# Optimization experiments

Measured on AMD Instinct MI355X. Metric: run time of the kernel, lower is better.

Reference implementation:

```python
import jax, jax.numpy as jnp
import numpy as np
from jax import lax

NUM_HEADS = 4
SIDE = 5  # side_dwconv


def setup_inputs() -> dict:
    key = jax.random.key(0)
    ks = jax.random.split(key, 7)
    B, C, H, W = 2, 128, 56, 56
    return {
        "x": jax.random.normal(ks[0], (B, C, H, W), dtype=jnp.float32),
        "qkv_w": jax.random.normal(ks[1], (3 * C, C), dtype=jnp.float32) * 0.02,
        "qkv_b": jax.random.normal(ks[2], (3 * C,), dtype=jnp.float32) * 0.02,
        "lepe_w": jax.random.normal(ks[3], (C, 1, SIDE, SIDE), dtype=jnp.float32) * 0.02,
        "lepe_b": jax.random.normal(ks[4], (C,), dtype=jnp.float32) * 0.02,
        "proj_w": jax.random.normal(ks[5], (C, C), dtype=jnp.float32) * 0.02,
        "proj_b": jax.random.normal(ks[6], (C,), dtype=jnp.float32) * 0.02,
    }


def reference(x, qkv_w, qkv_b, lepe_w, lepe_b, proj_w, proj_b):
    B, C, H, W = x.shape
    nh = NUM_HEADS
    hd = C // nh
    scale = hd ** (-0.5)
    N = H * W

    # 1x1 conv qkv == channel matmul
    qkv = jnp.einsum('oc,bchw->bohw', qkv_w, x) + qkv_b[None, :, None, None]
    q, k, v = jnp.split(qkv, 3, axis=1)  # each [B, C, H, W]

    qr = q.reshape(B, nh, hd, N)
    kr = k.reshape(B, nh, hd, N)
    vr = v.reshape(B, nh, hd, N)

    # attn = q^T k over head_dim -> [B, nh, N, N]
    attn = jnp.einsum('bhdn,bhdm->bhnm', qr, kr) * scale
    attn = jax.nn.softmax(attn, axis=-1)

    # out = attn @ v^T, then permute back to [B, C, H, W]
    out = jnp.einsum('bhnm,bhdm->bhdn', attn, vr).reshape(B, C, H, W)

    # depthwise LePE conv on v, fused with residual add
    pad = SIDE // 2
    lepe = lax.conv_general_dilated(
        v, lepe_w, window_strides=(1, 1), padding=[(pad, pad), (pad, pad)],
        dimension_numbers=('NCHW', 'OIHW', 'NCHW'), feature_group_count=C,
    ) + lepe_b[None, :, None, None]
    out = out + lepe

    # 1x1 conv proj
    out = jnp.einsum('oc,bchw->bohw', proj_w, out) + proj_b[None, :, None, None]
    return out
```

## Files before the change

kernel.cpp:

```cpp
#include <hip/hip_runtime.h>

typedef __bf16 bf16x8 __attribute__((ext_vector_type(8)));
typedef __bf16 bf16x4 __attribute__((ext_vector_type(4)));
typedef float  f32x4  __attribute__((ext_vector_type(4)));

#define NPIX  3136
#define WIMG  56
#define CCH   128
#define NH    4
#define HD    32
#define NSPLIT 4
#define QSCALE 0.2550565470841439f

#if __has_builtin(__builtin_amdgcn_exp2f)
#define FEXP2(x) __builtin_amdgcn_exp2f(x)
#else
#define FEXP2(x) __expf((x) * 0.6931471805599453f)
#endif


__device__ __forceinline__ int perm_inv(int k) {
    return (((k >> 5) & 1) * 2 + ((k >> 2) & 1)) * 16 + (((k >> 3) & 3) * 4) + (k & 3);
}

__global__ __launch_bounds__(256) void k_qkv(
    const float* __restrict__ x, const float* __restrict__ qkv_w,
    const float* __restrict__ qkv_b,
    __bf16* __restrict__ qT, __bf16* __restrict__ kT,
    __bf16* __restrict__ vT, __bf16* __restrict__ vP)
{
    __shared__ __bf16 xl[64][136];
    const int tid = threadIdx.x;
    const int w = tid >> 6, lane = tid & 63;
    const int col = lane & 15, g = lane >> 4;
    const int px0 = blockIdx.x * 64;
    const int slab = blockIdx.y;
    const int b = blockIdx.z;
    const int obase = slab * 128 + w * 32;

    {
        const int px = tid & 63, cq = tid >> 6;
        const float* xp = x + (size_t)b * CCH * NPIX + px0 + px;
        #pragma unroll
        for (int i = 0; i < 8; ++i) {
            const int c0 = cq * 4 + i * 16;
            const float v0 = xp[(size_t)(c0 + 0) * NPIX];
            const float v1 = xp[(size_t)(c0 + 1) * NPIX];
            const float v2 = xp[(size_t)(c0 + 2) * NPIX];
            const float v3 = xp[(size_t)(c0 + 3) * NPIX];
            bf16x4 bv = {(__bf16)v0, (__bf16)v1, (__bf16)v2, (__bf16)v3};
            *(bf16x4*)&xl[px][c0] = bv;
        }
    }
    __syncthreads();

    f32x4 acc[2][4];
    #pragma unroll
    for (int ot = 0; ot < 2; ++ot)
        #pragma unroll
        for (int a = 0; a < 4; ++a) acc[ot][a] = (f32x4){0.f, 0.f, 0.f, 0.f};

    #pragma unroll
    for (int ks = 0; ks < 4; ++ks) {
        const int c0 = ks * 32 + g * 8;
        #pragma unroll
        for (int ot = 0; ot < 2; ++ot) {
            const float* wrow = qkv_w + (size_t)(obase + ot * 16 + col) * CCH + c0;
            const float4 wA = *(const float4*)(wrow);
            const float4 wB = *(const float4*)(wrow + 4);
            bf16x8 af = {(__bf16)wA.x, (__bf16)wA.y, (__bf16)wA.z, (__bf16)wA.w,
                         (__bf16)wB.x, (__bf16)wB.y, (__bf16)wB.z, (__bf16)wB.w};
            #pragma unroll
            for (int a = 0; a < 4; ++a) {
                const bf16x8 bf_ = *(const bf16x8*)&xl[16 * a + col][c0];
                acc[ot][a] = __builtin_amdgcn_mfma_f32_16x16x32_bf16(af, bf_, acc[ot][a], 0, 0, 0);
            }
        }
    }

    #pragma unroll
    for (int ot = 0; ot < 2; ++ot) {
        const int orow = obase + ot * 16 + g * 4;
        const f32x4 bias4 = *(const f32x4*)(qkv_b + orow);
        if (slab == 0) {
            const int o = orow, h = o >> 5, d0 = o & 31;
            __bf16* dst = qT + ((size_t)(b * NH + h) * NPIX) * HD + d0;
            #pragma unroll
            for (int a = 0; a < 4; ++a) {
                const int px = px0 + 16 * a + col;
                bf16x4 v;
                #pragma unroll
                for (int r = 0; r < 4; ++r) v[r] = (__bf16)((acc[ot][a][r] + bias4[r]) * QSCALE);
                *(bf16x4*)(dst + (size_t)px * HD) = v;
            }
        } else if (slab == 1) {
            const int o = orow - 128, h = o >> 5, d0 = o & 31;
            __bf16* dst = kT + ((size_t)(b * NH + h) * NPIX) * HD + d0;
            #pragma unroll
            for (int a = 0; a < 4; ++a) {
                const int s = perm_inv(16 * a + col);
                bf16x4 v;
                #pragma unroll
                for (int r = 0; r < 4; ++r) v[r] = (__bf16)(acc[ot][a][r] + bias4[r]);
                *(bf16x4*)(dst + (size_t)(px0 + s) * HD) = v;
            }
        } else {
            const int c = orow - 256;
            #pragma unroll
            for (int a = 0; a < 4; ++a) {
                const int px = px0 + 16 * a + col;
                const int s = perm_inv(16 * a + col);
                bf16x4 v;
                #pragma unroll
                for (int r = 0; r < 4; ++r) v[r] = (__bf16)(acc[ot][a][r] + bias4[r]);
                *(bf16x4*)(vT + ((size_t)(b * NPIX + px)) * CCH + c) = v;
                #pragma unroll
                for (int r = 0; r < 4; ++r)
                    vP[((size_t)(b * CCH + c + r)) * NPIX + px0 + s] = v[r];
            }
        }
    }
}

__global__ __launch_bounds__(256) void k_attn(
    const __bf16* __restrict__ qT, const __bf16* __restrict__ kT,
    const __bf16* __restrict__ vP,
    __bf16* __restrict__ pO, float* __restrict__ pl)
{
    const int tid = threadIdx.x;
    const int w = tid >> 6, lane = tid & 63;
    const int col = lane & 15, g = lane >> 4;
    const int qt = blockIdx.x * 2 + (w >> 1);
    const int bh = blockIdx.y;
    const int sp = blockIdx.z * 2 + (w & 1);
    const int b = bh >> 2, h = bh & 3;
    const int qbase = qt * 32;
    const size_t headoff = (size_t)bh * NPIX * HD;
    const int c0h = h * HD;

    const bf16x8 aqA = *(const bf16x8*)(qT + headoff + (size_t)(qbase + col) * HD + g * 8);
    const bf16x8 aqB = *(const bf16x8*)(qT + headoff + (size_t)(qbase + 16 + col) * HD + g * 8);

    const __bf16 one = (__bf16)1.0f;
    const bf16x8 ones = {one, one, one, one, one, one, one, one};

    f32x4 O[2][2], Lacc[2];
    #pragma unroll
    for (int i = 0; i < 2; ++i) {
        Lacc[i] = (f32x4){0.f, 0.f, 0.f, 0.f};
        #pragma unroll
        for (int j = 0; j < 2; ++j) O[i][j] = (f32x4){0.f, 0.f, 0.f, 0.f};
    }

    const __bf16* kTh   = kT + headoff;
    const __bf16* vrow0 = vP + (size_t)(b * CCH + c0h + col)      * NPIX;
    const __bf16* vrow1 = vP + (size_t)(b * CCH + c0h + 16 + col) * NPIX;

    const int cs = (49 * sp) >> 2, ce = (49 * (sp + 1)) >> 2;
    const int nch = ce - cs;

#define LOADK(DK, CHUNK) do { const int _k0 = (CHUNK) * 64;                               \
        _Pragma("unroll")                                                                  \
        for (int _c = 0; _c < 4; ++_c)                                                     \
            DK[_c] = *(const bf16x8*)(kTh + (size_t)(_k0 + 16 * _c + col) * HD + g * 8);   \
        } while (0)

    auto compute = [&](const bf16x8* bk, int chunk) {
        const int k0 = chunk * 64;
        const bf16x8 vv00 = *(const bf16x8*)(vrow0 + k0      + g * 8);
        const bf16x8 vv01 = *(const bf16x8*)(vrow0 + k0 + 32 + g * 8);
        const bf16x8 vv10 = *(const bf16x8*)(vrow1 + k0      + g * 8);
        const bf16x8 vv11 = *(const bf16x8*)(vrow1 + k0 + 32 + g * 8);
        const f32x4 z = {0.f, 0.f, 0.f, 0.f};
        #pragma unroll
        for (int qh = 0; qh < 2; ++qh) {
            const bf16x8 aq = qh ? aqB : aqA;
            f32x4 s0 = __builtin_amdgcn_mfma_f32_16x16x32_bf16(bk[0], aq, z, 0, 0, 0);
            f32x4 s1 = __builtin_amdgcn_mfma_f32_16x16x32_bf16(bk[1], aq, z, 0, 0, 0);
            f32x4 s2 = __builtin_amdgcn_mfma_f32_16x16x32_bf16(bk[2], aq, z, 0, 0, 0);
            f32x4 s3 = __builtin_amdgcn_mfma_f32_16x16x32_bf16(bk[3], aq, z, 0, 0, 0);
            bf16x8 P0 = {(__bf16)FEXP2(s0[0]), (__bf16)FEXP2(s0[1]),
                         (__bf16)FEXP2(s0[2]), (__bf16)FEXP2(s0[3]),
                         (__bf16)FEXP2(s1[0]), (__bf16)FEXP2(s1[1]),
                         (__bf16)FEXP2(s1[2]), (__bf16)FEXP2(s1[3])};
            bf16x8 P1 = {(__bf16)FEXP2(s2[0]), (__bf16)FEXP2(s2[1]),
                         (__bf16)FEXP2(s2[2]), (__bf16)FEXP2(s2[3]),
                         (__bf16)FEXP2(s3[0]), (__bf16)FEXP2(s3[1]),
                         (__bf16)FEXP2(s3[2]), (__bf16)FEXP2(s3[3])};
            O[qh][0] = __builtin_amdgcn_mfma_f32_16x16x32_bf16(vv00, P0, O[qh][0], 0, 0, 0);
            O[qh][0] = __builtin_amdgcn_mfma_f32_16x16x32_bf16(vv01, P1, O[qh][0], 0, 0, 0);
            O[qh][1] = __builtin_amdgcn_mfma_f32_16x16x32_bf16(vv10, P0, O[qh][1], 0, 0, 0);
            O[qh][1] = __builtin_amdgcn_mfma_f32_16x16x32_bf16(vv11, P1, O[qh][1], 0, 0, 0);
            Lacc[qh] = __builtin_amdgcn_mfma_f32_16x16x32_bf16(ones, P0, Lacc[qh], 0, 0, 0);
            Lacc[qh] = __builtin_amdgcn_mfma_f32_16x16x32_bf16(ones, P1, Lacc[qh], 0, 0, 0);
        }
    };

    bf16x8 kA[4], kB[4];
    LOADK(kA, cs);
    int cc = cs;
    while (cc + 2 <= ce) {
        LOADK(kB, cc + 1);
        compute(kA, cc);
        LOADK(kA, (cc + 2 < ce) ? cc + 2 : cs);
        compute(kB, cc + 1);
        cc += 2;
    }
    if (cc < ce) compute(kA, cc);
#undef LOADK

    const int t = bh * 98 + qt;
    __bf16* po = pO + ((size_t)t * NSPLIT + sp) * 1024;
    #pragma unroll
    for (int qh = 0; qh < 2; ++qh)
        #pragma unroll
        for (int dh = 0; dh < 2; ++dh) {
            bf16x4 v = {(__bf16)O[qh][dh][0], (__bf16)O[qh][dh][1],
                        (__bf16)O[qh][dh][2], (__bf16)O[qh][dh][3]};
            *(bf16x4*)(po + (qh * 16 + col) * 32 + dh * 16 + g * 4) = v;
        }
    if (g == 0) {
        float* plp = pl + ((size_t)t * NSPLIT + sp) * 32;
        plp[col]      = Lacc[0][0];
        plp[col + 16] = Lacc[1][0];
    }
}

__global__ __launch_bounds__(256) void k_reduce(
    const __bf16* __restrict__ pO, const float* __restrict__ pl,
    const __bf16* __restrict__ vT,
    const float* __restrict__ lepe_w, const float* __restrict__ lepe_b,
    __bf16* __restrict__ attnT)
{
    __shared__ float wl[32][25];
    __shared__ float bl[32];
    const int tid = threadIdx.x;
    const int qt = blockIdx.x, bh = blockIdx.y;
    const int b = bh >> 2, h = bh & 3;
    const int c0h = h * HD;

    for (int i = tid; i < 800; i += 256) ((float*)wl)[i] = lepe_w[c0h * 25 + i];
    if (tid < 32) bl[tid] = lepe_b[c0h + tid];
    __syncthreads();

    const int q = tid >> 3;
    const int cq = (tid & 7) * 4;
    const size_t t = (size_t)bh * 98 + qt;

    float lt = 0.f;
    float o[4] = {0.f, 0.f, 0.f, 0.f};
    #pragma unroll
    for (int s = 0; s < NSPLIT; ++s) {
        lt += pl[(t * NSPLIT + s) * 32 + q];
        const bf16x4 pv = *(const bf16x4*)(pO + (t * NSPLIT + s) * 1024 + q * 32 + cq);
        #pragma unroll
        for (int i = 0; i < 4; ++i) o[i] += (float)pv[i];
    }
    const float linv = 1.0f / lt;
    #pragma unroll
    for (int i = 0; i < 4; ++i) o[i] = o[i] * linv + bl[cq + i];

    const int px = qt * 32 + q;
    const int py = px / WIMG, pxx = px % WIMG;
    const __bf16* vtb = vT + ((size_t)b * NPIX) * CCH + c0h + cq;
    #pragma unroll
    for (int dy = 0; dy < 5; ++dy) {
        const int yy = py + dy - 2;
        if (yy < 0 || yy >= WIMG) continue;
        #pragma unroll
        for (int dx = 0; dx < 5; ++dx) {
            const int xx = pxx + dx - 2;
            if (xx < 0 || xx >= WIMG) continue;
            const bf16x4 vv = *(const bf16x4*)(vtb + (size_t)(yy * WIMG + xx) * CCH);
            const int tap = dy * 5 + dx;
            #pragma unroll
            for (int i = 0; i < 4; ++i) o[i] += (float)vv[i] * wl[cq + i][tap];
        }
    }
    bf16x4 ov = {(__bf16)o[0], (__bf16)o[1], (__bf16)o[2], (__bf16)o[3]};
    *(bf16x4*)(attnT + ((size_t)(b * NPIX + px)) * CCH + c0h + cq) = ov;
}

__global__ __launch_bounds__(256) void k_proj(
    const __bf16* __restrict__ attnT, const float* __restrict__ proj_w,
    const float* __restrict__ proj_b, float* __restrict__ out)
{
    const int tid = threadIdx.x;
    const int w = tid >> 6, lane = tid & 63;
    const int col = lane & 15, g = lane >> 4;
    const int px0 = blockIdx.x * 32 + (w >> 1) * 16;
    const int obase = blockIdx.y * 32 + (w & 1) * 16;
    const int b = blockIdx.z;

    const float* wrow = proj_w + (size_t)(obase + col) * CCH;
    const __bf16* abase = attnT + (size_t)(b * NPIX + px0) * CCH;

    f32x4 acc = {0.f, 0.f, 0.f, 0.f};
    #pragma unroll
    for (int ks = 0; ks < 4; ++ks) {
        const int c0 = ks * 32 + g * 8;
        const float4 wA = *(const float4*)(wrow + c0);
        const float4 wB = *(const float4*)(wrow + c0 + 4);
        bf16x8 af = {(__bf16)wA.x, (__bf16)wA.y, (__bf16)wA.z, (__bf16)wA.w,
                     (__bf16)wB.x, (__bf16)wB.y, (__bf16)wB.z, (__bf16)wB.w};
        const bf16x8 bf_ = *(const bf16x8*)(abase + (size_t)col * CCH + c0);
        acc = __builtin_amdgcn_mfma_f32_16x16x32_bf16(af, bf_, acc, 0, 0, 0);
    }

    const f32x4 pb = *(const f32x4*)(proj_b + obase + g * 4);
    #pragma unroll
    for (int r = 0; r < 4; ++r)
        out[(size_t)(b * CCH + obase + g * 4 + r) * NPIX + px0 + col] = acc[r] + pb[r];
}

extern "C" void kernel_launch(void* const* d_in, const int* in_sizes, int n_in,
                              void* d_out, int out_size, void* d_ws, size_t ws_size,
                              hipStream_t stream)
{
    const float* x      = (const float*)d_in[0];
    const float* qkv_w  = (const float*)d_in[1];
    const float* qkv_b  = (const float*)d_in[2];
    const float* lepe_w = (const float*)d_in[3];
    const float* lepe_b = (const float*)d_in[4];
    const float* proj_w = (const float*)d_in[5];
    const float* proj_b = (const float*)d_in[6];
    float* out = (float*)d_out;

    char* p = (char*)d_ws;
    __bf16* qT    = (__bf16*)p;  p += (size_t)2 * NH * NPIX * HD * 2;
    __bf16* kT    = (__bf16*)p;  p += (size_t)2 * NH * NPIX * HD * 2;
    __bf16* vT    = (__bf16*)p;  p += (size_t)2 * NPIX * CCH * 2;
    __bf16* vP    = (__bf16*)p;  p += (size_t)2 * CCH * NPIX * 2;
    __bf16* attnT = (__bf16*)p;  p += (size_t)2 * NPIX * CCH * 2;
    __bf16* pO    = (__bf16*)p;  p += (size_t)784 * NSPLIT * 1024 * 2;
    float*  pl    = (float*)p;

    k_qkv   <<<dim3(49, 3, 2), dim3(256), 0, stream>>>(x, qkv_w, qkv_b, qT, kT, vT, vP);
    k_attn  <<<dim3(49, 8, 2), dim3(256), 0, stream>>>(qT, kT, vP, pO, pl);
    k_reduce<<<dim3(98, 8),    dim3(256), 0, stream>>>(pO, pl, vT, lepe_w, lepe_b, attnT);
    k_proj  <<<dim3(98, 4, 2), dim3(256), 0, stream>>>(attnT, proj_w, proj_b, out);
}
```

Baseline: 133.2 us.

## Give each attention wave 64 queries and split keys eight ways

Each wave in the attention kernel now handles 64 query rows instead of 32, so every loaded K and V fragment is reused across four query sub-tiles. The key range is split into eight parts instead of four, with the four waves of a block taking different splits, and the grid shape stays the same. The reduce kernel is reworked to match: each thread handles 8 channels with 8-wide vector loads, over 49 blocks per head. The aim is to cut K/V load traffic per MFMA, at the cost of more accumulator registers and twice as many partial results to reduce.

```diff
diff --git a/kernel.cpp b/kernel.cpp
--- a/kernel.cpp
+++ b/kernel.cpp
@@ -9,7 +9,7 @@
 #define CCH   128
 #define NH    4
 #define HD    32
-#define NSPLIT 4
+#define NSPLIT 8
 #define QSCALE 0.2550565470841439f
 
 #if __has_builtin(__builtin_amdgcn_exp2f)
@@ -130,100 +130,104 @@
     const int tid = threadIdx.x;
     const int w = tid >> 6, lane = tid & 63;
     const int col = lane & 15, g = lane >> 4;
-    const int qt = blockIdx.x * 2 + (w >> 1);
+    const int qt = blockIdx.x;
     const int bh = blockIdx.y;
-    const int sp = blockIdx.z * 2 + (w & 1);
+    const int sp = blockIdx.z * 4 + w;
     const int b = bh >> 2, h = bh & 3;
-    const int qbase = qt * 32;
+    const int qbase = qt * 64;
     const size_t headoff = (size_t)bh * NPIX * HD;
     const int c0h = h * HD;
 
-    const bf16x8 aqA = *(const bf16x8*)(qT + headoff + (size_t)(qbase + col) * HD + g * 8);
-    const bf16x8 aqB = *(const bf16x8*)(qT + headoff + (size_t)(qbase + 16 + col) * HD + g * 8);
+    const __bf16* qbp = qT + headoff + (size_t)(qbase + col) * HD + g * 8;
+    const bf16x8 aq0 = *(const bf16x8*)(qbp);
+    const bf16x8 aq1 = *(const bf16x8*)(qbp + 16 * HD);
+    const bf16x8 aq2 = *(const bf16x8*)(qbp + 32 * HD);
+    const bf16x8 aq3 = *(const bf16x8*)(qbp + 48 * HD);
 
     const __bf16 one = (__bf16)1.0f;
     const bf16x8 ones = {one, one, one, one, one, one, one, one};
 
-    f32x4 O[2][2], Lacc[2];
-    #pragma unroll
-    for (int i = 0; i < 2; ++i) {
-        Lacc[i] = (f32x4){0.f, 0.f, 0.f, 0.f};
-        #pragma unroll
-        for (int j = 0; j < 2; ++j) O[i][j] = (f32x4){0.f, 0.f, 0.f, 0.f};
-    }
+    f32x4 O00 = {0,0,0,0}, O01 = {0,0,0,0}, O10 = {0,0,0,0}, O11 = {0,0,0,0};
+    f32x4 O20 = {0,0,0,0}, O21 = {0,0,0,0}, O30 = {0,0,0,0}, O31 = {0,0,0,0};
+    f32x4 La0 = {0,0,0,0}, La1 = {0,0,0,0}, La2 = {0,0,0,0}, La3 = {0,0,0,0};
 
     const __bf16* kTh   = kT + headoff;
     const __bf16* vrow0 = vP + (size_t)(b * CCH + c0h + col)      * NPIX;
     const __bf16* vrow1 = vP + (size_t)(b * CCH + c0h + 16 + col) * NPIX;
 
-    const int cs = (49 * sp) >> 2, ce = (49 * (sp + 1)) >> 2;
-    const int nch = ce - cs;
-
-#define LOADK(DK, CHUNK) do { const int _k0 = (CHUNK) * 64;                               \
-        _Pragma("unroll")                                                                  \
-        for (int _c = 0; _c < 4; ++_c)                                                     \
-            DK[_c] = *(const bf16x8*)(kTh + (size_t)(_k0 + 16 * _c + col) * HD + g * 8);   \
-        } while (0)
-
-    auto compute = [&](const bf16x8* bk, int chunk) {
-        const int k0 = chunk * 64;
-        const bf16x8 vv00 = *(const bf16x8*)(vrow0 + k0      + g * 8);
-        const bf16x8 vv01 = *(const bf16x8*)(vrow0 + k0 + 32 + g * 8);
-        const bf16x8 vv10 = *(const bf16x8*)(vrow1 + k0      + g * 8);
-        const bf16x8 vv11 = *(const bf16x8*)(vrow1 + k0 + 32 + g * 8);
-        const f32x4 z = {0.f, 0.f, 0.f, 0.f};
-        #pragma unroll
-        for (int qh = 0; qh < 2; ++qh) {
-            const bf16x8 aq = qh ? aqB : aqA;
-            f32x4 s0 = __builtin_amdgcn_mfma_f32_16x16x32_bf16(bk[0], aq, z, 0, 0, 0);
-            f32x4 s1 = __builtin_amdgcn_mfma_f32_16x16x32_bf16(bk[1], aq, z, 0, 0, 0);
-            f32x4 s2 = __builtin_amdgcn_mfma_f32_16x16x32_bf16(bk[2], aq, z, 0, 0, 0);
-            f32x4 s3 = __builtin_amdgcn_mfma_f32_16x16x32_bf16(bk[3], aq, z, 0, 0, 0);
-            bf16x8 P0 = {(__bf16)FEXP2(s0[0]), (__bf16)FEXP2(s0[1]),
-                         (__bf16)FEXP2(s0[2]), (__bf16)FEXP2(s0[3]),
-                         (__bf16)FEXP2(s1[0]), (__bf16)FEXP2(s1[1]),
-                         (__bf16)FEXP2(s1[2]), (__bf16)FEXP2(s1[3])};
-            bf16x8 P1 = {(__bf16)FEXP2(s2[0]), (__bf16)FEXP2(s2[1]),
-                         (__bf16)FEXP2(s2[2]), (__bf16)FEXP2(s2[3]),
-                         (__bf16)FEXP2(s3[0]), (__bf16)FEXP2(s3[1]),
-                         (__bf16)FEXP2(s3[2]), (__bf16)FEXP2(s3[3])};
-            O[qh][0] = __builtin_amdgcn_mfma_f32_16x16x32_bf16(vv00, P0, O[qh][0], 0, 0, 0);
-            O[qh][0] = __builtin_amdgcn_mfma_f32_16x16x32_bf16(vv01, P1, O[qh][0], 0, 0, 0);
-            O[qh][1] = __builtin_amdgcn_mfma_f32_16x16x32_bf16(vv10, P0, O[qh][1], 0, 0, 0);
-            O[qh][1] = __builtin_amdgcn_mfma_f32_16x16x32_bf16(vv11, P1, O[qh][1], 0, 0, 0);
-            Lacc[qh] = __builtin_amdgcn_mfma_f32_16x16x32_bf16(ones, P0, Lacc[qh], 0, 0, 0);
-            Lacc[qh] = __builtin_amdgcn_mfma_f32_16x16x32_bf16(ones, P1, Lacc[qh], 0, 0, 0);
-        }
-    };
-
-    bf16x8 kA[4], kB[4];
-    LOADK(kA, cs);
+    const int cs = (49 * sp) >> 3, ce = (49 * (sp + 1)) >> 3;
+
+#define LOADK4(K0R, K1R, K2R, K3R, CHUNK) do { const int _k0 = (CHUNK) * 64;           \
+        K0R = *(const bf16x8*)(kTh + (size_t)(_k0      + col) * HD + g * 8);           \
+        K1R = *(const bf16x8*)(kTh + (size_t)(_k0 + 16 + col) * HD + g * 8);           \
+        K2R = *(const bf16x8*)(kTh + (size_t)(_k0 + 32 + col) * HD + g * 8);           \
+        K3R = *(const bf16x8*)(kTh + (size_t)(_k0 + 48 + col) * HD + g * 8); } while (0)
+
+#define SQH(AQ, O0R, O1R, LAR)  do {                                                   \
+        f32x4 s0 = __builtin_amdgcn_mfma_f32_16x16x32_bf16(ck0, AQ, zz, 0, 0, 0);      \
+        f32x4 s1 = __builtin_amdgcn_mfma_f32_16x16x32_bf16(ck1, AQ, zz, 0, 0, 0);      \
+        f32x4 s2 = __builtin_amdgcn_mfma_f32_16x16x32_bf16(ck2, AQ, zz, 0, 0, 0);      \
+        f32x4 s3 = __builtin_amdgcn_mfma_f32_16x16x32_bf16(ck3, AQ, zz, 0, 0, 0);      \
+        bf16x8 P0 = {(__bf16)FEXP2(s0[0]), (__bf16)FEXP2(s0[1]),                       \
+                     (__bf16)FEXP2(s0[2]), (__bf16)FEXP2(s0[3]),                       \
+                     (__bf16)FEXP2(s1[0]), (__bf16)FEXP2(s1[1]),                       \
+                     (__bf16)FEXP2(s1[2]), (__bf16)FEXP2(s1[3])};                      \
+        bf16x8 P1 = {(__bf16)FEXP2(s2[0]), (__bf16)FEXP2(s2[1]),                       \
+                     (__bf16)FEXP2(s2[2]), (__bf16)FEXP2(s2[3]),                       \
+                     (__bf16)FEXP2(s3[0]), (__bf16)FEXP2(s3[1]),                       \
+                     (__bf16)FEXP2(s3[2]), (__bf16)FEXP2(s3[3])};                      \
+        O0R = __builtin_amdgcn_mfma_f32_16x16x32_bf16(vv00, P0, O0R, 0, 0, 0);         \
+        O0R = __builtin_amdgcn_mfma_f32_16x16x32_bf16(vv01, P1, O0R, 0, 0, 0);         \
+        O1R = __builtin_amdgcn_mfma_f32_16x16x32_bf16(vv10, P0, O1R, 0, 0, 0);         \
+        O1R = __builtin_amdgcn_mfma_f32_16x16x32_bf16(vv11, P1, O1R, 0, 0, 0);         \
+        LAR = __builtin_amdgcn_mfma_f32_16x16x32_bf16(ones, P0, LAR, 0, 0, 0);         \
+        LAR = __builtin_amdgcn_mfma_f32_16x16x32_bf16(ones, P1, LAR, 0, 0, 0);         \
+    } while (0)
+
+#define CHUNK_STEP(K0R, K1R, K2R, K3R, CHUNK) do {                                     \
+        const int _kv0 = (CHUNK) * 64;                                                 \
+        const bf16x8 vv00 = *(const bf16x8*)(vrow0 + _kv0      + g * 8);               \
+        const bf16x8 vv01 = *(const bf16x8*)(vrow0 + _kv0 + 32 + g * 8);               \
+        const bf16x8 vv10 = *(const bf16x8*)(vrow1 + _kv0      + g * 8);               \
+        const bf16x8 vv11 = *(const bf16x8*)(vrow1 + _kv0 + 32 + g * 8);               \
+        const bf16x8 ck0 = K0R, ck1 = K1R, ck2 = K2R, ck3 = K3R;                       \
+        const f32x4 zz = {0.f, 0.f, 0.f, 0.f};                                         \
+        SQH(aq0, O00, O01, La0);                                                       \
+        SQH(aq1, O10, O11, La1);                                                       \
+        SQH(aq2, O20, O21, La2);                                                       \
+        SQH(aq3, O30, O31, La3);                                                       \
+    } while (0)
+
+    bf16x8 ka0, ka1, ka2, ka3, kb0, kb1, kb2, kb3;
+    LOADK4(ka0, ka1, ka2, ka3, cs);
     int cc = cs;
     while (cc + 2 <= ce) {
-        LOADK(kB, cc + 1);
-        compute(kA, cc);
-        LOADK(kA, (cc + 2 < ce) ? cc + 2 : cs);
-        compute(kB, cc + 1);
+        LOADK4(kb0, kb1, kb2, kb3, cc + 1);
+        CHUNK_STEP(ka0, ka1, ka2, ka3, cc);
+        LOADK4(ka0, ka1, ka2, ka3, (cc + 2 < ce) ? cc + 2 : cs);
+        CHUNK_STEP(kb0, kb1, kb2, kb3, cc + 1);
         cc += 2;
     }
-    if (cc < ce) compute(kA, cc);
-#undef LOADK
-
-    const int t = bh * 98 + qt;
-    __bf16* po = pO + ((size_t)t * NSPLIT + sp) * 1024;
-    #pragma unroll
-    for (int qh = 0; qh < 2; ++qh)
-        #pragma unroll
-        for (int dh = 0; dh < 2; ++dh) {
-            bf16x4 v = {(__bf16)O[qh][dh][0], (__bf16)O[qh][dh][1],
-                        (__bf16)O[qh][dh][2], (__bf16)O[qh][dh][3]};
-            *(bf16x4*)(po + (qh * 16 + col) * 32 + dh * 16 + g * 4) = v;
-        }
-    if (g == 0) {
-        float* plp = pl + ((size_t)t * NSPLIT + sp) * 32;
-        plp[col]      = Lacc[0][0];
-        plp[col + 16] = Lacc[1][0];
-    }
+    if (cc < ce) CHUNK_STEP(ka0, ka1, ka2, ka3, cc);
+#undef LOADK4
+#undef SQH
+#undef CHUNK_STEP
+
+    const int t = bh * 49 + qt;
+    __bf16* po = pO + ((size_t)t * NSPLIT + sp) * 64 * 32;
+    float* plp = pl + ((size_t)t * NSPLIT + sp) * 64;
+#define STQH(QH, O0R, O1R, LAR) do {                                                   \
+        bf16x4 v0 = {(__bf16)O0R[0], (__bf16)O0R[1], (__bf16)O0R[2], (__bf16)O0R[3]};  \
+        bf16x4 v1 = {(__bf16)O1R[0], (__bf16)O1R[1], (__bf16)O1R[2], (__bf16)O1R[3]};  \
+        *(bf16x4*)(po + ((QH) * 16 + col) * 32      + g * 4) = v0;                     \
+        *(bf16x4*)(po + ((QH) * 16 + col) * 32 + 16 + g * 4) = v1;                     \
+        if (g == 0) plp[(QH) * 16 + col] = LAR[0];                                     \
+    } while (0)
+    STQH(0, O00, O01, La0);
+    STQH(1, O10, O11, La1);
+    STQH(2, O20, O21, La2);
+    STQH(3, O30, O31, La3);
+#undef STQH
 }
 
 __global__ __launch_bounds__(256) void k_reduce(
@@ -243,26 +247,26 @@
     if (tid < 32) bl[tid] = lepe_b[c0h + tid];
     __syncthreads();
 
-    const int q = tid >> 3;
-    const int cq = (tid & 7) * 4;
-    const size_t t = (size_t)bh * 98 + qt;
+    const int q  = tid >> 2;
+    const int dg = (tid & 3) * 8;
+    const size_t t = (size_t)bh * 49 + qt;
 
     float lt = 0.f;
-    float o[4] = {0.f, 0.f, 0.f, 0.f};
+    float o[8] = {0.f, 0.f, 0.f, 0.f, 0.f, 0.f, 0.f, 0.f};
     #pragma unroll
     for (int s = 0; s < NSPLIT; ++s) {
-        lt += pl[(t * NSPLIT + s) * 32 + q];
-        const bf16x4 pv = *(const bf16x4*)(pO + (t * NSPLIT + s) * 1024 + q * 32 + cq);
-        #pragma unroll
-        for (int i = 0; i < 4; ++i) o[i] += (float)pv[i];
+        lt += pl[(t * NSPLIT + s) * 64 + q];
+        const bf16x8 pv = *(const bf16x8*)(pO + ((t * NSPLIT + s) * 64 + q) * 32 + dg);
+        #pragma unroll
+        for (int i = 0; i < 8; ++i) o[i] += (float)pv[i];
     }
     const float linv = 1.0f / lt;
     #pragma unroll
-    for (int i = 0; i < 4; ++i) o[i] = o[i] * linv + bl[cq + i];
-
-    const int px = qt * 32 + q;
+    for (int i = 0; i < 8; ++i) o[i] = o[i] * linv + bl[dg + i];
+
+    const int px = qt * 64 + q;
     const int py = px / WIMG, pxx = px % WIMG;
-    const __bf16* vtb = vT + ((size_t)b * NPIX) * CCH + c0h + cq;
+    const __bf16* vtb = vT + ((size_t)b * NPIX) * CCH + c0h + dg;
     #pragma unroll
     for (int dy = 0; dy < 5; ++dy) {
         const int yy = py + dy - 2;
@@ -271,14 +275,15 @@
         for (int dx = 0; dx < 5; ++dx) {
             const int xx = pxx + dx - 2;
             if (xx < 0 || xx >= WIMG) continue;
-            const bf16x4 vv = *(const bf16x4*)(vtb + (size_t)(yy * WIMG + xx) * CCH);
+            const bf16x8 vv = *(const bf16x8*)(vtb + (size_t)(yy * WIMG + xx) * CCH);
             const int tap = dy * 5 + dx;
             #pragma unroll
-            for (int i = 0; i < 4; ++i) o[i] += (float)vv[i] * wl[cq + i][tap];
+            for (int i = 0; i < 8; ++i) o[i] += (float)vv[i] * wl[dg + i][tap];
         }
     }
-    bf16x4 ov = {(__bf16)o[0], (__bf16)o[1], (__bf16)o[2], (__bf16)o[3]};
-    *(bf16x4*)(attnT + ((size_t)(b * NPIX + px)) * CCH + c0h + cq) = ov;
+    bf16x8 ov = {(__bf16)o[0], (__bf16)o[1], (__bf16)o[2], (__bf16)o[3],
+                 (__bf16)o[4], (__bf16)o[5], (__bf16)o[6], (__bf16)o[7]};
+    *(bf16x8*)(attnT + ((size_t)(b * NPIX + px)) * CCH + c0h + dg) = ov;
 }
 
 __global__ __launch_bounds__(256) void k_proj(
@@ -332,11 +337,11 @@
     __bf16* vT    = (__bf16*)p;  p += (size_t)2 * NPIX * CCH * 2;
     __bf16* vP    = (__bf16*)p;  p += (size_t)2 * CCH * NPIX * 2;
     __bf16* attnT = (__bf16*)p;  p += (size_t)2 * NPIX * CCH * 2;
-    __bf16* pO    = (__bf16*)p;  p += (size_t)784 * NSPLIT * 1024 * 2;
+    __bf16* pO    = (__bf16*)p;  p += (size_t)392 * NSPLIT * 64 * 32 * 2;
     float*  pl    = (float*)p;
 
     k_qkv   <<<dim3(49, 3, 2), dim3(256), 0, stream>>>(x, qkv_w, qkv_b, qT, kT, vT, vP);
     k_attn  <<<dim3(49, 8, 2), dim3(256), 0, stream>>>(qT, kT, vP, pO, pl);
-    k_reduce<<<dim3(98, 8),    dim3(256), 0, stream>>>(pO, pl, vT, lepe_w, lepe_b, attnT);
+    k_reduce<<<dim3(49, 8),    dim3(256), 0, stream>>>(pO, pl, vT, lepe_w, lepe_b, attnT);
     k_proj  <<<dim3(98, 4, 2), dim3(256), 0, stream>>>(attnT, proj_w, proj_b, out);
 }
```

After: 123.2 us. 1.08x faster.
